# Kernel tuning notes

Measured on AMD Instinct MI355X. Metric: run time of the kernel, lower is better.

## Reference

```python
import jax, jax.numpy as jnp
import numpy as np

B, L, D, H, F, NL, K, G = 2, 2048, 768, 12, 3072, 12, 128, 16
HD = D // H
SCALE = HD ** -0.5


def setup_inputs() -> dict:
    key = jax.random.key(0)
    ks = jax.random.split(key, 8)
    n = lambda k, s, std=0.02: jax.random.normal(k, s, dtype=jnp.float32) * std
    return {
        "x": jax.random.normal(ks[0], (B, L, D), dtype=jnp.float32),
        "pos_conv_w": n(ks[1], (D, D // G, K)),
        "pos_conv_b": jnp.zeros((D,), jnp.float32),
        "ln0_g": jnp.ones((D,), jnp.float32), "ln0_b": jnp.zeros((D,), jnp.float32),
        "Wq": n(ks[2], (NL, D, D)), "bq": jnp.zeros((NL, D), jnp.float32),
        "Wk": n(ks[3], (NL, D, D)), "bk": jnp.zeros((NL, D), jnp.float32),
        "Wv": n(ks[4], (NL, D, D)), "bv": jnp.zeros((NL, D), jnp.float32),
        "Wo": n(ks[5], (NL, D, D)), "bo": jnp.zeros((NL, D), jnp.float32),
        "ln1_g": jnp.ones((NL, D), jnp.float32), "ln1_b": jnp.zeros((NL, D), jnp.float32),
        "W1": n(ks[6], (NL, D, F)), "b1": jnp.zeros((NL, F), jnp.float32),
        "W2": n(ks[7], (NL, F, D)), "b2": jnp.zeros((NL, D), jnp.float32),
        "ln2_g": jnp.ones((NL, D), jnp.float32), "ln2_b": jnp.zeros((NL, D), jnp.float32),
    }


def _ln(x, g, b, eps=1e-5):
    m = jnp.mean(x, axis=-1, keepdims=True)
    v = jnp.mean(jnp.square(x - m), axis=-1, keepdims=True)
    return (x - m) * jax.lax.rsqrt(v + eps) * g + b


def reference(x, pos_conv_w, pos_conv_b, ln0_g, ln0_b, Wq, bq, Wk, bk, Wv, bv, Wo, bo,
              ln1_g, ln1_b, W1, b1, W2, b2, ln2_g, ln2_b):
    b_, l_, d_ = x.shape
    # positional grouped conv embedding (kernel even -> drop last frame), GELU, residual add
    pos = jax.lax.conv_general_dilated(x.transpose(0, 2, 1), pos_conv_w, (1,), [(K // 2, K // 2)],
                                       feature_group_count=G)  # (B, D, L+1)
    pos = pos[:, :, :l_] + pos_conv_b[None, :, None]
    h = x + jax.nn.gelu(pos, approximate=False).transpose(0, 2, 1)
    # post-norm encoder (layer_norm_first=False): LN applied before the layer stack
    h = _ln(h, ln0_g, ln0_b)

    def layer(h, p):
        wq, bq_, wk, bk_, wv, bv_, wo, bo_, g1, be1, w1, bf1, w2, bf2, g2, be2 = p
        r = h
        q = (h @ wq + bq_).reshape(b_, l_, H, HD)
        k = (h @ wk + bk_).reshape(b_, l_, H, HD)
        v = (h @ wv + bv_).reshape(b_, l_, H, HD)
        w = jax.nn.softmax(SCALE * jnp.einsum('blhd,bmhd->bhlm', q, k), axis=-1)
        o = jnp.einsum('bhlm,bmhd->blhd', w, v).reshape(b_, l_, d_)
        h = r + (o @ wo + bo_)
        h = _ln(h, g1, be1)
        ff = jax.nn.gelu(h @ w1 + bf1, approximate=False) @ w2 + bf2
        h = _ln(h + ff, g2, be2)
        return h, None

    h, _ = jax.lax.scan(layer, h, (Wq, bq, Wk, bk, Wv, bv, Wo, bo,
                                   ln1_g, ln1_b, W1, b1, W2, b2, ln2_g, ln2_b))
    return h
```

## Files before the change

kernel.cpp:

```cpp
#include <hip/hip_runtime.h>
#include <hip/hip_bf16.h>
#include <stdint.h>

#define B_ 2
#define L_ 2048
#define D_ 768
#define H_ 12
#define F_ 3072
#define NL_ 12
#define K_ 128
#define G_ 16
#define HD_ 64
#define CPG_ 48
#define M_TOK (B_*L_)
#define SCALE_ 0.125f

typedef __hip_bfloat16 bf16;
typedef __bf16 bf16x8 __attribute__((ext_vector_type(8)));
typedef float f32x4 __attribute__((ext_vector_type(4)));

__device__ __forceinline__ void gload16(const void* g, void* l) {
  __builtin_amdgcn_global_load_lds((const __attribute__((address_space(1))) void*)g,
                                   (__attribute__((address_space(3))) void*)l, 16, 0, 0);
}

__global__ __launch_bounds__(256) void convw_kernel(const float* __restrict__ w,
                                                    bf16* __restrict__ wT2) {
  int idx = blockIdx.x * 256 + threadIdx.x;
  int ci = idx & 63;
  int row = idx >> 6;
  int d = row % 48;
  int t2 = row / 48;
  int kk = t2 & 127;
  int g = t2 >> 7;
  float v = (ci < 48) ? w[(((size_t)(g * 48 + d) * 48) + ci) * 128 + kk] : 0.f;
  wT2[idx] = __float2bfloat16(v);
}

__global__ __launch_bounds__(256) void conv_mfma(const float* __restrict__ x,
                                                 const bf16* __restrict__ wT2,
                                                 const float* __restrict__ bias,
                                                 float* __restrict__ out) {
  int flat = blockIdx.x;
  int wgid = (flat & 7) * 64 + (flat >> 3);
  const int g = wgid >> 5;
  int rem = wgid & 31;
  const int l0 = (rem & 15) * 128;
  const int b = rem >> 4;

  const int tid = threadIdx.x, w = tid >> 6, lane = tid & 63;
  const int c15 = lane & 15, g4 = lane >> 4;
  __shared__ __align__(16) bf16 win[256 * 64];
  __shared__ __align__(16) bf16 Wl[2 * 48 * 64];

  {
    int lg = l0 - 64 + tid;
    char* dst = (char*)win + tid * 128;
    int swr = (tid & 7) << 4;
    uint4 z4 = {0u, 0u, 0u, 0u};
    if ((unsigned)lg < 2048u) {
      const float* srow = x + ((size_t)(b * 2048 + lg) * 768 + g * 48);
#pragma unroll
      for (int c = 0; c < 6; ++c) {
        float4 v0 = *(const float4*)(srow + c * 8);
        float4 v1 = *(const float4*)(srow + c * 8 + 4);
        union { bf16 h[8]; uint4 u; } uu;
        uu.h[0] = __float2bfloat16(v0.x); uu.h[1] = __float2bfloat16(v0.y);
        uu.h[2] = __float2bfloat16(v0.z); uu.h[3] = __float2bfloat16(v0.w);
        uu.h[4] = __float2bfloat16(v1.x); uu.h[5] = __float2bfloat16(v1.y);
        uu.h[6] = __float2bfloat16(v1.z); uu.h[7] = __float2bfloat16(v1.w);
        *(uint4*)(dst + ((c * 16) ^ swr)) = uu.u;
      }
    } else {
#pragma unroll
      for (int c = 0; c < 6; ++c) *(uint4*)(dst + ((c * 16) ^ swr)) = z4;
    }
    *(uint4*)(dst + (96 ^ swr)) = z4;
    *(uint4*)(dst + (112 ^ swr)) = z4;
  }
  __syncthreads();

  f32x4 acc[2][3];
  const f32x4 vzero = {0.f, 0.f, 0.f, 0.f};
#pragma unroll
  for (int i = 0; i < 2; ++i)
#pragma unroll
    for (int j = 0; j < 3; ++j) acc[i][j] = vzero;

  const char* wbase = (const char*)wT2 + (size_t)g * 128 * 48 * 128;

  for (int kp = 0; kp < 64; ++kp) {
#pragma unroll
    for (int i = 0; i < 3; ++i) {
      int coff = w * 3072 + i * 1024;
      int c = coff + (lane << 4);
      int row96 = c >> 7;
      int s = row96 / 48;
      int d = row96 - s * 48;
      int cb2 = c & 127;
      gload16(wbase + ((size_t)((2 * kp + s) * 48 + d)) * 128 + (cb2 ^ ((d & 7) << 4)),
              (char*)Wl + coff);
    }
    __syncthreads();
#pragma unroll
    for (int s = 0; s < 2; ++s) {
      int kk = 2 * kp + s;
#pragma unroll
      for (int cb = 0; cb < 2; ++cb) {
        int a0r = w * 16 + c15 + kk;
        int a1r = 64 + a0r;
        bf16x8 a0 = *(const bf16x8*)((const char*)win + a0r * 128 + ((cb * 64 + g4 * 16) ^ ((a0r & 7) << 4)));
        bf16x8 a1 = *(const bf16x8*)((const char*)win + a1r * 128 + ((cb * 64 + g4 * 16) ^ ((a1r & 7) << 4)));
#pragma unroll
        for (int ct = 0; ct < 3; ++ct) {
          int d = ct * 16 + c15;
          bf16x8 bfrag = *(const bf16x8*)((const char*)Wl + s * 6144 + d * 128 +
                                          ((cb * 64 + g4 * 16) ^ ((d & 7) << 4)));
          acc[0][ct] = __builtin_amdgcn_mfma_f32_16x16x32_bf16(a0, bfrag, acc[0][ct], 0, 0, 0);
          acc[1][ct] = __builtin_amdgcn_mfma_f32_16x16x32_bf16(a1, bfrag, acc[1][ct], 0, 0, 0);
        }
      }
    }
    __syncthreads();
  }

#pragma unroll
  for (int ls = 0; ls < 2; ++ls)
#pragma unroll
    for (int ct = 0; ct < 3; ++ct) {
      int dg = g * 48 + ct * 16 + c15;
      float bv = bias[dg];
#pragma unroll
      for (int r = 0; r < 4; ++r) {
        int l = l0 + ls * 64 + w * 16 + g4 * 4 + r;
        size_t idx = (size_t)(b * 2048 + l) * 768 + dg;
        float vv = acc[ls][ct][r] + bv;
        vv = 0.5f * vv * (1.0f + erff(vv * 0.70710678f));
        out[idx] = x[idx] + vv;
      }
    }
}

__global__ __launch_bounds__(256) void ln_kernel(const float* __restrict__ a,
                                                 const float* __restrict__ r,
                                                 const float* __restrict__ g,
                                                 const float* __restrict__ be,
                                                 float* __restrict__ out,
                                                 bf16* __restrict__ outb) {
  int w = threadIdx.x >> 6, lane = threadIdx.x & 63;
  size_t row = (size_t)blockIdx.x * 4 + w;
  const float* ar = a + row * 768;
  const float* rr = r ? r + row * 768 : nullptr;
  float4 v[3];
  float s = 0.f;
#pragma unroll
  for (int i = 0; i < 3; ++i) {
    int c = lane * 4 + i * 256;
    float4 vv = *(const float4*)(ar + c);
    if (rr) {
      float4 rv = *(const float4*)(rr + c);
      vv.x += rv.x; vv.y += rv.y; vv.z += rv.z; vv.w += rv.w;
    }
    v[i] = vv;
    s += vv.x + vv.y + vv.z + vv.w;
  }
#pragma unroll
  for (int st = 1; st < 64; st <<= 1) s += __shfl_xor(s, st);
  float mean = s * (1.0f / 768.0f);
  float s2 = 0.f;
#pragma unroll
  for (int i = 0; i < 3; ++i) {
    float dx = v[i].x - mean, dy = v[i].y - mean, dz = v[i].z - mean, dw = v[i].w - mean;
    s2 += dx * dx + dy * dy + dz * dz + dw * dw;
  }
#pragma unroll
  for (int st = 1; st < 64; st <<= 1) s2 += __shfl_xor(s2, st);
  float rstd = rsqrtf(s2 * (1.0f / 768.0f) + 1e-5f);
#pragma unroll
  for (int i = 0; i < 3; ++i) {
    int c = lane * 4 + i * 256;
    float4 gv = *(const float4*)(g + c);
    float4 bv = *(const float4*)(be + c);
    float4 ov;
    ov.x = (v[i].x - mean) * rstd * gv.x + bv.x;
    ov.y = (v[i].y - mean) * rstd * gv.y + bv.y;
    ov.z = (v[i].z - mean) * rstd * gv.z + bv.z;
    ov.w = (v[i].w - mean) * rstd * gv.w + bv.w;
    *(float4*)(out + row * 768 + c) = ov;
    if (outb) {
      union { bf16 h[4]; uint2 u; } pk;
      pk.h[0] = __float2bfloat16(ov.x); pk.h[1] = __float2bfloat16(ov.y);
      pk.h[2] = __float2bfloat16(ov.z); pk.h[3] = __float2bfloat16(ov.w);
      *(uint2*)(outb + row * 768 + c) = pk.u;
    }
  }
}

__global__ __launch_bounds__(256) void prep_weights(const float* __restrict__ WqB,
                                                    const float* __restrict__ WkB,
                                                    const float* __restrict__ WvB,
                                                    const float* __restrict__ WoB,
                                                    const float* __restrict__ W1B,
                                                    const float* __restrict__ W2B,
                                                    const float* __restrict__ bqB,
                                                    const float* __restrict__ bkB,
                                                    const float* __restrict__ bvB,
                                                    bf16* __restrict__ wqkvb,
                                                    bf16* __restrict__ wob,
                                                    bf16* __restrict__ w1b,
                                                    bf16* __restrict__ w2b,
                                                    float* __restrict__ bqkv,
                                                    int l) {
  __shared__ float t[32][33];
  int tid = threadIdx.x;
  int tx = tid & 31, ty = tid >> 5;
  const float* wq = WqB + (size_t)l * 768 * 768;
  const float* wk = WkB + (size_t)l * 768 * 768;
  const float* wv = WvB + (size_t)l * 768 * 768;
  const float* wo = WoB + (size_t)l * 768 * 768;
  const float* w1 = W1B + (size_t)l * 768 * 3072;
  const float* w2 = W2B + (size_t)l * 3072 * 768;

  int blk = blockIdx.x;
  if (blk >= 6912) {
    int i = (blk - 6912) * 256 + tid;
    if (i < 2304)
      bqkv[i] = (i < 768) ? bqB[(size_t)l * 768 + i]
              : (i < 1536) ? bkB[(size_t)l * 768 + i - 768]
                           : bvB[(size_t)l * 768 + i - 1536];
    return;
  }
  if (blk < 1728) {
    int n0 = (blk % 72) * 32, k0 = (blk / 72) * 32;
    const float* src = (n0 < 768) ? wq : (n0 < 1536) ? wk : wv;
    int nn = (n0 >= 1536) ? (n0 - 1536) : (n0 >= 768 ? n0 - 768 : n0);
#pragma unroll
    for (int i = 0; i < 32; i += 8) t[ty + i][tx] = src[(size_t)(k0 + ty + i) * 768 + nn + tx];
    __syncthreads();
#pragma unroll
    for (int i = 0; i < 32; i += 8)
      wqkvb[(size_t)(n0 + ty + i) * 768 + k0 + tx] = __float2bfloat16(t[tx][ty + i]);
    return;
  }
  blk -= 1728;
  if (blk < 576) {
    int c0 = (blk % 24) * 32, r0 = (blk / 24) * 32;
#pragma unroll
    for (int i = 0; i < 32; i += 8) t[ty + i][tx] = wo[(size_t)(r0 + ty + i) * 768 + c0 + tx];
    __syncthreads();
#pragma unroll
    for (int i = 0; i < 32; i += 8)
      wob[(size_t)(c0 + ty + i) * 768 + r0 + tx] = __float2bfloat16(t[tx][ty + i]);
    return;
  }
  blk -= 576;
  if (blk < 2304) {
    int c0 = (blk % 96) * 32, r0 = (blk / 96) * 32;
#pragma unroll
    for (int i = 0; i < 32; i += 8) t[ty + i][tx] = w1[(size_t)(r0 + ty + i) * 3072 + c0 + tx];
    __syncthreads();
#pragma unroll
    for (int i = 0; i < 32; i += 8)
      w1b[(size_t)(c0 + ty + i) * 768 + r0 + tx] = __float2bfloat16(t[tx][ty + i]);
    return;
  }
  blk -= 2304;
  {
    int c0 = (blk % 24) * 32, r0 = (blk / 24) * 32;
#pragma unroll
    for (int i = 0; i < 32; i += 8) t[ty + i][tx] = w2[(size_t)(r0 + ty + i) * 768 + c0 + tx];
    __syncthreads();
#pragma unroll
    for (int i = 0; i < 32; i += 8)
      w2b[(size_t)(c0 + ty + i) * 3072 + r0 + tx] = __float2bfloat16(t[tx][ty + i]);
  }
}

template <int BM, int BN, int GELU, int BF16OUT, int VOUT = 0>
__global__ __launch_bounds__(256) void gemm_bf16(const bf16* __restrict__ A,
                                                 const bf16* __restrict__ BT,
                                                 const float* __restrict__ bias,
                                                 void* __restrict__ Cout,
                                                 int N, int Kd,
                                                 bf16* __restrict__ vTout = nullptr) {
  constexpr int WM = BM / 2, MF = WM / 16;
  constexpr int WN = BN / 2, FN = WN / 16;
  __shared__ bf16 As[BM * 64];
  __shared__ bf16 Bs[BN * 64];
  const int tid = threadIdx.x, w = tid >> 6, lane = tid & 63;
  int gx = gridDim.x;
  int flat = blockIdx.x + gx * blockIdx.y;
  int cpx = (gx * gridDim.y) >> 3;
  int sw = (flat & 7) * cpx + (flat >> 3);
  const int bn = sw % gx, bm = sw / gx;
  const int wr = w >> 1, wc = w & 1;
  const int c15 = lane & 15, g4 = lane >> 4;
  const int lrow8 = lane >> 3;
  const int cb = (lane & 7) * 16;

  f32x4 acc[MF][FN];
  const f32x4 vzero = {0.f, 0.f, 0.f, 0.f};
#pragma unroll
  for (int i = 0; i < MF; ++i)
#pragma unroll
    for (int j = 0; j < FN; ++j) acc[i][j] = vzero;

  const char* Ab = (const char*)A;
  const char* Bb = (const char*)BT;

  for (int k0 = 0; k0 < Kd; k0 += 64) {
#pragma unroll
    for (int i = 0; i < BM / 32; ++i) {
      int t = w + 4 * i;
      int row = t * 8 + lrow8;
      gload16(Ab + ((size_t)(bm * BM + row) * Kd + k0) * 2 + (cb ^ ((row & 7) << 4)),
              (char*)As + t * 1024);
    }
#pragma unroll
    for (int i = 0; i < BN / 32; ++i) {
      int t = w + 4 * i;
      int row = t * 8 + lrow8;
      gload16(Bb + ((size_t)(bn * BN + row) * Kd + k0) * 2 + (cb ^ ((row & 7) << 4)),
              (char*)Bs + t * 1024);
    }
    __syncthreads();
    bf16x8 af[MF][2], bfr[FN][2];
#pragma unroll
    for (int kf = 0; kf < 2; ++kf) {
      int kbyte = kf * 64 + g4 * 16;
#pragma unroll
      for (int mf = 0; mf < MF; ++mf) {
        int row = wr * WM + mf * 16 + c15;
        af[mf][kf] = *(const bf16x8*)((const char*)As + row * 128 + (kbyte ^ ((row & 7) << 4)));
      }
#pragma unroll
      for (int fn = 0; fn < FN; ++fn) {
        int row = wc * WN + fn * 16 + c15;
        bfr[fn][kf] = *(const bf16x8*)((const char*)Bs + row * 128 + (kbyte ^ ((row & 7) << 4)));
      }
    }
    __builtin_amdgcn_s_setprio(1);
#pragma unroll
    for (int mf = 0; mf < MF; ++mf)
#pragma unroll
      for (int fn = 0; fn < FN; ++fn) {
        acc[mf][fn] = __builtin_amdgcn_mfma_f32_16x16x32_bf16(af[mf][0], bfr[fn][0], acc[mf][fn], 0, 0, 0);
        acc[mf][fn] = __builtin_amdgcn_mfma_f32_16x16x32_bf16(af[mf][1], bfr[fn][1], acc[mf][fn], 0, 0, 0);
      }
    __builtin_amdgcn_s_setprio(0);
    __syncthreads();
  }
#pragma unroll
  for (int fn = 0; fn < FN; ++fn) {
    int col = bn * BN + wc * WN + fn * 16 + c15;
    float bv = bias[col];
#pragma unroll
    for (int mf = 0; mf < MF; ++mf) {
#pragma unroll
      for (int r = 0; r < 4; ++r) {
        int row = bm * BM + wr * WM + mf * 16 + g4 * 4 + r;
        float vv = acc[mf][fn][r] + bv;
        if (GELU) vv = 0.5f * vv * (1.0f + erff(vv * 0.70710678f));
        if (BF16OUT) {
          if (VOUT && col >= 1536) {
            int hd2 = col - 1536, hh = hd2 >> 6, dd = hd2 & 63;
            int bb = row >> 11, ll = row & 2047;
            vTout[((size_t)((bb * 12 + hh) * 64 + dd) << 11) + ll] = __float2bfloat16(vv);
          } else {
            ((bf16*)Cout)[(size_t)row * N + col] = __float2bfloat16(vv);
          }
        } else {
          ((float*)Cout)[(size_t)row * N + col] = vv;
        }
      }
    }
  }
}

__global__ __launch_bounds__(256) void attn_mfma(const bf16* __restrict__ qkv,
                                                 const bf16* __restrict__ vT,
                                                 bf16* __restrict__ ob) {
  int bid = blockIdx.x + 32 * (blockIdx.y + 12 * blockIdx.z);
  int wgid = (bid & 7) * 96 + (bid >> 3);
  const int q0 = (wgid & 31) * 64;
  int bh = wgid >> 5;
  const int h = bh % 12, b = bh / 12;

  const int tid = threadIdx.x, w = tid >> 6, lane = tid & 63;
  const int c15 = lane & 15, g4 = lane >> 4;
  const int lrow8 = lane >> 3;
  const int cb = (lane & 7) * 16;
  __shared__ bf16 Kl[2][4096];
  __shared__ bf16 Vl[2][4096];
  __shared__ bf16 Pl[4096];

  const f32x4 vzero = {0.f, 0.f, 0.f, 0.f};
  const char* qp = (const char*)qkv + (((size_t)(b * 2048 + q0 + w * 16 + c15)) * 2304 + h * 64) * 2;
  bf16x8 qa0 = *(const bf16x8*)(qp + g4 * 16);
  bf16x8 qa1 = *(const bf16x8*)(qp + 64 + g4 * 16);

  bf16x8 b_one;
#pragma unroll
  for (int i = 0; i < 8; ++i) b_one[i] = (__bf16)1.0f;

  f32x4 o[4], o5;
#pragma unroll
  for (int i = 0; i < 4; ++i) o[i] = vzero;
  o5 = vzero;
  float m = -1e30f;
  const float SC2 = 0.18033688f;
  const float THR = 11.54f;

  const char* kgb = (const char*)qkv + (((size_t)(b * 2048)) * 2304 + 768 + h * 64) * 2;
  const char* vgb = (const char*)vT + ((size_t)((b * 12 + h) * 64) * 2048) * 2;
  char* Plw = (char*)Pl + w * 2048;

  const int rr0 = w * 8 + lrow8;
  const int swz = cb ^ (lrow8 << 4);
  const char* ka0 = kgb + (size_t)rr0 * 4608 + swz;
  const char* ka1 = ka0 + 32 * 4608;
  const char* va0 = vgb + (size_t)rr0 * 4096 + swz;
  const char* va1 = va0 + 32 * 4096;
  char* kd0 = (char*)Kl[0] + w * 1024;
  char* vd0 = (char*)Vl[0] + w * 1024;

#define STAGE(kt, bufi)                                                        \
  {                                                                            \
    size_t ko = (size_t)(kt) * 294912;                                         \
    size_t vo = (size_t)(kt) * 128;                                            \
    int lo = (bufi) * 8192;                                                    \
    gload16(ka0 + ko, kd0 + lo);                                               \
    gload16(ka1 + ko, kd0 + lo + 4096);                                        \
    gload16(va0 + vo, vd0 + lo);                                               \
    gload16(va1 + vo, vd0 + lo + 4096);                                        \
  }

  STAGE(0, 0);
  __syncthreads();

  for (int kt = 0; kt < 32; ++kt) {
    int cur = kt & 1;
    if (kt + 1 < 32) STAGE(kt + 1, cur ^ 1);

    const char* Kc = (const char*)Kl[cur];
    const char* Vc = (const char*)Vl[cur];

    f32x4 sc[4];
    __builtin_amdgcn_s_setprio(1);
#pragma unroll
    for (int fn = 0; fn < 4; ++fn) {
      int key = fn * 16 + c15;
      const char* kr = Kc + key * 128;
      int sw = (key & 7) << 4;
      bf16x8 kb0 = *(const bf16x8*)(kr + ((g4 * 16) ^ sw));
      bf16x8 kb1 = *(const bf16x8*)(kr + ((64 + g4 * 16) ^ sw));
      f32x4 s = __builtin_amdgcn_mfma_f32_16x16x32_bf16(kb0, qa0, vzero, 0, 0, 0);
      s = __builtin_amdgcn_mfma_f32_16x16x32_bf16(kb1, qa1, s, 0, 0, 0);
      sc[fn] = s;
    }
    __builtin_amdgcn_s_setprio(0);

    float pm = fmaxf(
        fmaxf(fmaxf(fmaxf(sc[0][0], sc[0][1]), fmaxf(sc[0][2], sc[0][3])),
              fmaxf(fmaxf(sc[1][0], sc[1][1]), fmaxf(sc[1][2], sc[1][3]))),
        fmaxf(fmaxf(fmaxf(sc[2][0], sc[2][1]), fmaxf(sc[2][2], sc[2][3])),
              fmaxf(fmaxf(sc[3][0], sc[3][1]), fmaxf(sc[3][2], sc[3][3]))));
    int ok = (pm * SC2 <= m + THR) ? 1 : 0;

    if (!__all(ok)) {
      float tm = pm;
      tm = fmaxf(tm, __shfl_xor(tm, 16));
      tm = fmaxf(tm, __shfl_xor(tm, 32));
      float mn = fmaxf(m, tm * SC2);
      float alpha = exp2f(m - mn);
      m = mn;
#pragma unroll
      for (int r = 0; r < 4; ++r) {
        float ar = __shfl(alpha, g4 * 4 + r);
        o[0][r] *= ar; o[1][r] *= ar; o[2][r] *= ar; o[3][r] *= ar;
        o5[r] *= ar;
      }
    }

    {
      char* prow = Plw + c15 * 128;
      int swp = (c15 & 7) << 4;
#pragma unroll
      for (int fn = 0; fn < 4; ++fn) {
        union { bf16 hh[4]; uint2 u; } pk;
#pragma unroll
        for (int r = 0; r < 4; ++r)
          pk.hh[r] = __float2bfloat16(exp2f(fmaf(sc[fn][r], SC2, -m)));
        *(uint2*)(prow + ((fn * 32 + g4 * 8) ^ swp)) = pk.u;
      }
    }

    {
      const char* pr = Plw + c15 * 128;
      int sw = (c15 & 7) << 4;
      bf16x8 pa0 = *(const bf16x8*)(pr + ((g4 * 16) ^ sw));
      bf16x8 pa1 = *(const bf16x8*)(pr + ((64 + g4 * 16) ^ sw));
      __builtin_amdgcn_s_setprio(1);
#pragma unroll
      for (int fh = 0; fh < 4; ++fh) {
        int hd = fh * 16 + c15;
        const char* vr = Vc + hd * 128;
        int swv = (hd & 7) << 4;
        bf16x8 vb0 = *(const bf16x8*)(vr + ((g4 * 16) ^ swv));
        bf16x8 vb1 = *(const bf16x8*)(vr + ((64 + g4 * 16) ^ swv));
        o[fh] = __builtin_amdgcn_mfma_f32_16x16x32_bf16(pa0, vb0, o[fh], 0, 0, 0);
        o[fh] = __builtin_amdgcn_mfma_f32_16x16x32_bf16(pa1, vb1, o[fh], 0, 0, 0);
      }
      o5 = __builtin_amdgcn_mfma_f32_16x16x32_bf16(pa0, b_one, o5, 0, 0, 0);
      o5 = __builtin_amdgcn_mfma_f32_16x16x32_bf16(pa1, b_one, o5, 0, 0, 0);
      __builtin_amdgcn_s_setprio(0);
    }
    __syncthreads();
  }
#undef STAGE

#pragma unroll
  for (int r = 0; r < 4; ++r) {
    float inv = 1.0f / o5[r];
    size_t row = (size_t)(b * 2048 + q0 + w * 16 + g4 * 4 + r);
#pragma unroll
    for (int fh = 0; fh < 4; ++fh)
      ob[row * 768 + h * 64 + fh * 16 + c15] = __float2bfloat16(o[fh][r] * inv);
  }
}

extern "C" void kernel_launch(void* const* d_in, const int* in_sizes, int n_in,
                              void* d_out, int out_size, void* d_ws, size_t ws_size,
                              hipStream_t stream) {
  const float* x      = (const float*)d_in[0];
  const float* pcw    = (const float*)d_in[1];
  const float* pcb    = (const float*)d_in[2];
  const float* ln0_g  = (const float*)d_in[3];
  const float* ln0_b  = (const float*)d_in[4];
  const float* Wq     = (const float*)d_in[5];
  const float* bq     = (const float*)d_in[6];
  const float* Wk     = (const float*)d_in[7];
  const float* bk     = (const float*)d_in[8];
  const float* Wv     = (const float*)d_in[9];
  const float* bv     = (const float*)d_in[10];
  const float* Wo     = (const float*)d_in[11];
  const float* bo     = (const float*)d_in[12];
  const float* ln1_g  = (const float*)d_in[13];
  const float* ln1_b  = (const float*)d_in[14];
  const float* W1     = (const float*)d_in[15];
  const float* b1     = (const float*)d_in[16];
  const float* W2     = (const float*)d_in[17];
  const float* b2     = (const float*)d_in[18];
  const float* ln2_g  = (const float*)d_in[19];
  const float* ln2_b  = (const float*)d_in[20];

  const size_t MDB = (size_t)M_TOK * D_ * 4;
  char* W = (char*)d_ws;
  float* h    = (float*)W;
  float* tmp  = (float*)(W + MDB);
  char*  big  = W + 2 * MDB;
  bf16*  qkv  = (bf16*)big;
  bf16*  ff   = (bf16*)big;
  bf16*  wT2  = (bf16*)big;
  char* p = W + 2 * MDB + 25165824;
  bf16* h_bf  = (bf16*)p; p += (size_t)M_TOK * D_ * 2;
  bf16* obuf  = (bf16*)p; p += (size_t)M_TOK * D_ * 2;
  bf16* vT    = (bf16*)p; p += (size_t)M_TOK * D_ * 2;
  bf16* wqkvb = (bf16*)p; p += (size_t)2304 * 768 * 2;
  bf16* wob   = (bf16*)p; p += (size_t)768 * 768 * 2;
  bf16* w1b   = (bf16*)p; p += (size_t)3072 * 768 * 2;
  bf16* w2b   = (bf16*)p; p += (size_t)768 * 3072 * 2;
  float* bqkv = (float*)p;

  convw_kernel<<<24576, 256, 0, stream>>>(pcw, wT2);
  conv_mfma<<<512, 256, 0, stream>>>(x, wT2, pcb, tmp);
  ln_kernel<<<M_TOK / 4, 256, 0, stream>>>(tmp, nullptr, ln0_g, ln0_b, h, h_bf);

  for (int l = 0; l < NL_; ++l) {
    prep_weights<<<6921, 256, 0, stream>>>(Wq, Wk, Wv, Wo, W1, W2, bq, bk, bv,
                                           wqkvb, wob, w1b, w2b, bqkv, l);

    gemm_bf16<128, 128, 0, 1, 1><<<dim3(18, 32), 256, 0, stream>>>(h_bf, wqkvb, bqkv, qkv, 2304, 768, vT);
    attn_mfma<<<dim3(32, 12, 2), 256, 0, stream>>>(qkv, vT, obuf);
    gemm_bf16<64, 64, 0, 0><<<dim3(12, 64), 256, 0, stream>>>(obuf, wob, bo + (size_t)l * D_, tmp, 768, 768);
    ln_kernel<<<M_TOK / 4, 256, 0, stream>>>(tmp, h, ln1_g + (size_t)l * D_, ln1_b + (size_t)l * D_, h, h_bf);
    gemm_bf16<128, 128, 1, 1><<<dim3(24, 32), 256, 0, stream>>>(h_bf, w1b, b1 + (size_t)l * F_, ff, 3072, 768);
    gemm_bf16<64, 64, 0, 0><<<dim3(12, 64), 256, 0, stream>>>(ff, w2b, b2 + (size_t)l * D_, tmp, 768, 3072);
    float* out_ln2 = (l == NL_ - 1) ? (float*)d_out : h;
    ln_kernel<<<M_TOK / 4, 256, 0, stream>>>(tmp, h, ln2_g + (size_t)l * D_, ln2_b + (size_t)l * D_, out_ln2, h_bf);
  }
}
```

Baseline: 2.411 ms.

## Keep residual stream and GEMM outputs in bf16, drop fp32 hidden state

After: 2.277 ms. 5.6% less time.

```diff
diff --git a/kernel.cpp b/kernel.cpp
--- a/kernel.cpp
+++ b/kernel.cpp
@@ -142,25 +142,18 @@
 }
 
 __global__ __launch_bounds__(256) void ln_kernel(const float* __restrict__ a,
-                                                 const float* __restrict__ r,
                                                  const float* __restrict__ g,
                                                  const float* __restrict__ be,
-                                                 float* __restrict__ out,
                                                  bf16* __restrict__ outb) {
   int w = threadIdx.x >> 6, lane = threadIdx.x & 63;
   size_t row = (size_t)blockIdx.x * 4 + w;
   const float* ar = a + row * 768;
-  const float* rr = r ? r + row * 768 : nullptr;
   float4 v[3];
   float s = 0.f;
 #pragma unroll
   for (int i = 0; i < 3; ++i) {
     int c = lane * 4 + i * 256;
     float4 vv = *(const float4*)(ar + c);
-    if (rr) {
-      float4 rv = *(const float4*)(rr + c);
-      vv.x += rv.x; vv.y += rv.y; vv.z += rv.z; vv.w += rv.w;
-    }
     v[i] = vv;
     s += vv.x + vv.y + vv.z + vv.w;
   }
@@ -181,17 +174,71 @@
     int c = lane * 4 + i * 256;
     float4 gv = *(const float4*)(g + c);
     float4 bv = *(const float4*)(be + c);
-    float4 ov;
-    ov.x = (v[i].x - mean) * rstd * gv.x + bv.x;
-    ov.y = (v[i].y - mean) * rstd * gv.y + bv.y;
-    ov.z = (v[i].z - mean) * rstd * gv.z + bv.z;
-    ov.w = (v[i].w - mean) * rstd * gv.w + bv.w;
-    *(float4*)(out + row * 768 + c) = ov;
-    if (outb) {
-      union { bf16 h[4]; uint2 u; } pk;
-      pk.h[0] = __float2bfloat16(ov.x); pk.h[1] = __float2bfloat16(ov.y);
-      pk.h[2] = __float2bfloat16(ov.z); pk.h[3] = __float2bfloat16(ov.w);
-      *(uint2*)(outb + row * 768 + c) = pk.u;
+    union { bf16 h[4]; uint2 u; } pk;
+    pk.h[0] = __float2bfloat16((v[i].x - mean) * rstd * gv.x + bv.x);
+    pk.h[1] = __float2bfloat16((v[i].y - mean) * rstd * gv.y + bv.y);
+    pk.h[2] = __float2bfloat16((v[i].z - mean) * rstd * gv.z + bv.z);
+    pk.h[3] = __float2bfloat16((v[i].w - mean) * rstd * gv.w + bv.w);
+    *(uint2*)(outb + row * 768 + c) = pk.u;
+  }
+}
+
+template <int F32OUT>
+__global__ __launch_bounds__(256) void ln_bf(const bf16* __restrict__ a,
+                                             const bf16* __restrict__ r,
+                                             const float* __restrict__ g,
+                                             const float* __restrict__ be,
+                                             bf16* __restrict__ outb,
+                                             float* __restrict__ outf) {
+  int w = threadIdx.x >> 6, lane = threadIdx.x & 63;
+  size_t row = (size_t)blockIdx.x * 4 + w;
+  const bf16* ar = a + row * 768;
+  const bf16* rr = r + row * 768;
+  float v[3][4];
+  float s = 0.f;
+#pragma unroll
+  for (int i = 0; i < 3; ++i) {
+    int c = lane * 4 + i * 256;
+    union { uint2 u; uint16_t h[4]; } ua, urr;
+    ua.u = *(const uint2*)(ar + c);
+    urr.u = *(const uint2*)(rr + c);
+#pragma unroll
+    for (int j = 0; j < 4; ++j) {
+      float x = __uint_as_float((uint32_t)ua.h[j] << 16) +
+                __uint_as_float((uint32_t)urr.h[j] << 16);
+      v[i][j] = x; s += x;
+    }
+  }
+#pragma unroll
+  for (int st = 1; st < 64; st <<= 1) s += __shfl_xor(s, st);
+  float mean = s * (1.0f / 768.0f);
+  float s2 = 0.f;
+#pragma unroll
+  for (int i = 0; i < 3; ++i)
+#pragma unroll
+    for (int j = 0; j < 4; ++j) {
+      float d2 = v[i][j] - mean;
+      s2 += d2 * d2;
+    }
+#pragma unroll
+  for (int st = 1; st < 64; st <<= 1) s2 += __shfl_xor(s2, st);
+  float rstd = rsqrtf(s2 * (1.0f / 768.0f) + 1e-5f);
+#pragma unroll
+  for (int i = 0; i < 3; ++i) {
+    int c = lane * 4 + i * 256;
+    float4 gv = *(const float4*)(g + c);
+    float4 bv = *(const float4*)(be + c);
+    float o0 = (v[i][0] - mean) * rstd * gv.x + bv.x;
+    float o1 = (v[i][1] - mean) * rstd * gv.y + bv.y;
+    float o2 = (v[i][2] - mean) * rstd * gv.z + bv.z;
+    float o3 = (v[i][3] - mean) * rstd * gv.w + bv.w;
+    union { bf16 h[4]; uint2 u; } pk;
+    pk.h[0] = __float2bfloat16(o0); pk.h[1] = __float2bfloat16(o1);
+    pk.h[2] = __float2bfloat16(o2); pk.h[3] = __float2bfloat16(o3);
+    *(uint2*)(outb + row * 768 + c) = pk.u;
+    if (F32OUT) {
+      float4 of = {o0, o1, o2, o3};
+      *(float4*)(outf + row * 768 + c) = of;
     }
   }
 }
@@ -556,12 +603,12 @@
 
   const size_t MDB = (size_t)M_TOK * D_ * 4;
   char* W = (char*)d_ws;
-  float* h    = (float*)W;
   float* tmp  = (float*)(W + MDB);
   char*  big  = W + 2 * MDB;
   bf16*  qkv  = (bf16*)big;
   bf16*  ff   = (bf16*)big;
   bf16*  wT2  = (bf16*)big;
+  bf16*  tmp_bf = (bf16*)W;
   char* p = W + 2 * MDB + 25165824;
   bf16* h_bf  = (bf16*)p; p += (size_t)M_TOK * D_ * 2;
   bf16* obuf  = (bf16*)p; p += (size_t)M_TOK * D_ * 2;
@@ -574,7 +621,7 @@
 
   convw_kernel<<<24576, 256, 0, stream>>>(pcw, wT2);
   conv_mfma<<<512, 256, 0, stream>>>(x, wT2, pcb, tmp);
-  ln_kernel<<<M_TOK / 4, 256, 0, stream>>>(tmp, nullptr, ln0_g, ln0_b, h, h_bf);
+  ln_kernel<<<M_TOK / 4, 256, 0, stream>>>(tmp, ln0_g, ln0_b, h_bf);
 
   for (int l = 0; l < NL_; ++l) {
     prep_weights<<<6921, 256, 0, stream>>>(Wq, Wk, Wv, Wo, W1, W2, bq, bk, bv,
@@ -582,11 +629,13 @@
 
     gemm_bf16<128, 128, 0, 1, 1><<<dim3(18, 32), 256, 0, stream>>>(h_bf, wqkvb, bqkv, qkv, 2304, 768, vT);
     attn_mfma<<<dim3(32, 12, 2), 256, 0, stream>>>(qkv, vT, obuf);
-    gemm_bf16<64, 64, 0, 0><<<dim3(12, 64), 256, 0, stream>>>(obuf, wob, bo + (size_t)l * D_, tmp, 768, 768);
-    ln_kernel<<<M_TOK / 4, 256, 0, stream>>>(tmp, h, ln1_g + (size_t)l * D_, ln1_b + (size_t)l * D_, h, h_bf);
+    gemm_bf16<64, 64, 0, 1><<<dim3(12, 64), 256, 0, stream>>>(obuf, wob, bo + (size_t)l * D_, tmp_bf, 768, 768);
+    ln_bf<0><<<M_TOK / 4, 256, 0, stream>>>(tmp_bf, h_bf, ln1_g + (size_t)l * D_, ln1_b + (size_t)l * D_, h_bf, nullptr);
     gemm_bf16<128, 128, 1, 1><<<dim3(24, 32), 256, 0, stream>>>(h_bf, w1b, b1 + (size_t)l * F_, ff, 3072, 768);
-    gemm_bf16<64, 64, 0, 0><<<dim3(12, 64), 256, 0, stream>>>(ff, w2b, b2 + (size_t)l * D_, tmp, 768, 3072);
-    float* out_ln2 = (l == NL_ - 1) ? (float*)d_out : h;
-    ln_kernel<<<M_TOK / 4, 256, 0, stream>>>(tmp, h, ln2_g + (size_t)l * D_, ln2_b + (size_t)l * D_, out_ln2, h_bf);
-  }
-}
+    gemm_bf16<64, 64, 0, 1><<<dim3(12, 64), 256, 0, stream>>>(ff, w2b, b2 + (size_t)l * D_, tmp_bf, 768, 3072);
+    if (l == NL_ - 1)
+      ln_bf<1><<<M_TOK / 4, 256, 0, stream>>>(tmp_bf, h_bf, ln2_g + (size_t)l * D_, ln2_b + (size_t)l * D_, h_bf, (float*)d_out);
+    else
+      ln_bf<0><<<M_TOK / 4, 256, 0, stream>>>(tmp_bf, h_bf, ln2_g + (size_t)l * D_, ln2_b + (size_t)l * D_, h_bf, nullptr);
+  }
+}
```
